# Kernel optimization log

Hardware: AMD Instinct MI355X
Metric: run time of the kernel (lower is better)

Reference implementation:

```python
import jax, jax.numpy as jnp
import numpy as np

BS, NUM_VISIT, MAX_FEAT, MAX_TARGET = 32, 6, 12, 16
NUM_FEAT, NUM_REL, HIDDEN, REDUCED, OUT = 1992, 11, 128, 256, 90
GAMMA = 0.1


def setup_inputs() -> dict:
    key = jax.random.key(0)
    ks = jax.random.split(key, 20)
    u = lambda k, shape: jax.random.uniform(k, shape, dtype=jnp.float32)
    # one/multi-hot-like dense float inputs (per docstring)
    feat_index = (u(ks[0], (BS, NUM_VISIT, MAX_FEAT, NUM_FEAT)) < 0.01).astype(jnp.float32)
    neighbor_index = (u(ks[1], (BS, NUM_VISIT, MAX_FEAT, MAX_TARGET, NUM_FEAT)) < 0.001).astype(jnp.float32)
    rel_index = (u(ks[2], (BS, NUM_VISIT, MAX_FEAT, MAX_TARGET, NUM_REL)) < 0.2).astype(jnp.float32)
    # parameters (torch.rand init in the original; xavier for embedding)
    bound = float(np.sqrt(6.0 / (NUM_FEAT + HIDDEN)))
    emb_weight = jax.random.uniform(ks[3], (NUM_FEAT, HIDDEN), dtype=jnp.float32, minval=-bound, maxval=bound)
    return {
        "feat_index": feat_index,
        "neighbor_index": neighbor_index,
        "rel_index": rel_index,
        "emb_weight": emb_weight,
        "W_edge": u(ks[4], (NUM_REL, HIDDEN)),
        "W_v": u(ks[5], (REDUCED, HIDDEN)),
        "W_r": u(ks[6], (REDUCED, HIDDEN)),
        "b_v": u(ks[7], (REDUCED,)),
        "b_r": u(ks[8], (REDUCED,)),
        "W_alpha": u(ks[9], (NUM_FEAT,)),
        "b_alpha": u(ks[10], (MAX_FEAT,)),
        "W_beta": u(ks[11], (MAX_FEAT,)),
        "b_beta": u(ks[12], (NUM_VISIT,)),
        "W_l": u(ks[13], (REDUCED, REDUCED)),
        "b_l": u(ks[14], (REDUCED,)),
        "fc_W": u(ks[15], (OUT, 2 * REDUCED)) * 0.05,
        "fc_b": u(ks[16], (OUT,)) * 0.05,
    }


def reference(feat_index, neighbor_index, rel_index, emb_weight, W_edge, W_v, W_r,
              b_v, b_r, W_alpha, b_alpha, W_beta, b_beta, W_l, b_l, fc_W, fc_b):
    num_visit = feat_index.shape[1]
    # decay buffer lamb[i] = exp(-gamma*(num_visit - i))
    lamb = jnp.exp(-GAMMA * (num_visit - jnp.arange(num_visit, dtype=feat_index.dtype)))

    # node-level attention alpha: (b,v,m)
    alpha = jax.nn.softmax(jnp.einsum('n,bvmn->bvm', W_alpha, feat_index) + b_alpha)
    # visit-level attention beta: (b,v), modulated by temporal decay
    beta = jnp.tanh(jnp.einsum('m,bvm->bv', W_beta, alpha) + b_beta) * lamb

    # reduced node embeddings: (num_feat, reduced)
    reduced_emb = emb_weight @ W_v.T + b_v
    # attention-weighted neighbor aggregation; sum over targets t fused in
    attn = alpha * beta[:, :, None]                       # (b,v,m)
    node_agg = jnp.einsum('bvm,bvmtn,nr->bvmr', attn, neighbor_index, reduced_emb)

    # reduced edge (relation) embeddings: (num_rel, reduced)
    reduced_edge = W_edge @ W_r.T + b_r
    edge_agg = jnp.einsum('bvmtr,rd->bvmd', rel_index, reduced_edge)  # sum over t fused

    agg = node_agg + edge_agg                             # (b,v,m,reduced)
    # einsum('dd, bvfd -> bvfd') in torch takes the diagonal of W_l
    h = jax.nn.relu(jnp.diagonal(W_l) * agg + b_l)        # (b,v,m,reduced)

    h_g = h.sum(axis=(1, 2))                              # (b, reduced)
    # einsum('bvmn,bvmr->bvnr').sum(n).sum(v) == contract over v,m,n
    h_p = jnp.einsum('bvm,bvmr->br', feat_index.sum(-1), h)

    z_joint = jnp.concatenate([h_g, h_p], axis=-1)        # (b, 2*reduced)
    return jax.nn.sigmoid(z_joint @ fc_W.T + fc_b)
```

## Files before the change

kernel.cpp:

```cpp
#include <hip/hip_runtime.h>
#include <math.h>

#define BS   32
#define NV   6
#define MF   12
#define MT   16
#define NF   1992
#define NR   11
#define HID  128
#define RED  256
#define OUTD 90
#define GAMMA 0.1f

#define WS_HG    0
#define WS_HP    (WS_HG + BS*RED)
#define WS_ATTN  (WS_HP + BS*RED)
#define WS_FSUM  (WS_ATTN + BS*NV*MF)
#define WS_REMB  (WS_FSUM + BS*NV*MF)
#define WS_REDGE (WS_REMB + NF*RED)
#define WS_WTV   (WS_REDGE + NR*RED)
#define WS_WTR   (WS_WTV + HID*RED)
#define WS_FCWT  (WS_WTR + HID*RED)

#define N_WTV  (HID*RED)
#define N_WTR  (HID*RED)
#define N_FCWT (2*RED*OUTD)
#define PREP_ELEMS (N_WTV + N_WTR + N_FCWT)
#define PREP_BLOCKS ((PREP_ELEMS + 255) / 256)

__global__ __launch_bounds__(256) void k_prep_attn(
        const float* __restrict__ W_v, const float* __restrict__ W_r,
        const float* __restrict__ fc_W,
        const float* __restrict__ feat, const float* __restrict__ W_alpha,
        const float* __restrict__ b_alpha, const float* __restrict__ W_beta,
        const float* __restrict__ b_beta,
        float* __restrict__ WT_v, float* __restrict__ WT_r, float* __restrict__ fcWT,
        float* __restrict__ attn_ws, float* __restrict__ fsum_ws) {
    int blk = blockIdx.x;
    int tid = threadIdx.x;
    if (blk < PREP_BLOCKS) {
        int i = blk * 256 + tid;
        if (i < N_WTV) {
            int k = i >> 8, r = i & 255;
            WT_v[i] = W_v[r * HID + k];
        } else if (i < N_WTV + N_WTR) {
            int j = i - N_WTV;
            int k = j >> 8, r = j & 255;
            WT_r[j] = W_r[r * HID + k];
        } else if (i < PREP_ELEMS) {
            int j = i - (N_WTV + N_WTR);
            int jj = j / OUTD, o = j - jj * OUTD;
            fcWT[j] = fc_W[o * (2 * RED) + jj];
        }
        return;
    }
    int bv   = blk - PREP_BLOCKS;
    int v    = bv % NV;
    int wave = tid >> 6;
    int lane = tid & 63;
    __shared__ float dot12[MF], fs12[MF];
    const float* base = feat + (size_t)bv * MF * NF;
    for (int m = wave; m < MF; m += 4) {
        const float4* rw = (const float4*)(base + (size_t)m * NF);
        const float4* wa = (const float4*)W_alpha;
        float da = 0.f, fs = 0.f;
        for (int i = lane; i < NF / 4; i += 64) {
            float4 x = rw[i];
            float4 w = wa[i];
            da += w.x * x.x + w.y * x.y + w.z * x.z + w.w * x.w;
            fs += x.x + x.y + x.z + x.w;
        }
        #pragma unroll
        for (int off = 32; off > 0; off >>= 1) {
            da += __shfl_xor(da, off);
            fs += __shfl_xor(fs, off);
        }
        if (lane == 0) { dot12[m] = da; fs12[m] = fs; }
    }
    __syncthreads();
    if (tid == 0) {
        float logits[MF];
        float mx = -1e30f;
        for (int m = 0; m < MF; ++m) { logits[m] = dot12[m] + b_alpha[m]; mx = fmaxf(mx, logits[m]); }
        float s = 0.f;
        for (int m = 0; m < MF; ++m) { logits[m] = expf(logits[m] - mx); s += logits[m]; }
        float inv = 1.f / s;
        float bdot = 0.f;
        for (int m = 0; m < MF; ++m) { logits[m] *= inv; bdot += W_beta[m] * logits[m]; }
        float lamb = expf(-GAMMA * (float)(NV - v));
        float beta = tanhf(bdot + b_beta[v]) * lamb;
        for (int m = 0; m < MF; ++m) {
            attn_ws[bv * MF + m] = logits[m] * beta;
            fsum_ws[bv * MF + m] = fs12[m];
        }
    }
}

#define NPB 4
#define NODE_BLOCKS (NF / NPB)
__global__ __launch_bounds__(256) void k_reduce(
        const float* __restrict__ emb, const float* __restrict__ W_edge,
        const float* __restrict__ WT_v, const float* __restrict__ WT_r,
        const float* __restrict__ b_v, const float* __restrict__ b_r,
        float* __restrict__ remb, float* __restrict__ redge) {
    int blk = blockIdx.x;
    int tid = threadIdx.x;
    if (blk < NODE_BLOCKS) {
        __shared__ float rows[NPB][HID];
        int n0 = blk * NPB;
        for (int i = tid; i < NPB * HID; i += 256)
            rows[i >> 7][i & 127] = emb[(size_t)n0 * HID + i];
        __syncthreads();
        float bv0 = b_v[tid];
        float a0 = bv0, a1 = bv0, a2 = bv0, a3 = bv0;
        #pragma unroll 4
        for (int k = 0; k < HID; ++k) {
            float w = WT_v[k * RED + tid];
            a0 += rows[0][k] * w;
            a1 += rows[1][k] * w;
            a2 += rows[2][k] * w;
            a3 += rows[3][k] * w;
        }
        remb[(size_t)(n0 + 0) * RED + tid] = a0;
        remb[(size_t)(n0 + 1) * RED + tid] = a1;
        remb[(size_t)(n0 + 2) * RED + tid] = a2;
        remb[(size_t)(n0 + 3) * RED + tid] = a3;
    } else {
        int e = blk - NODE_BLOCKS;
        __shared__ float row[HID];
        if (tid < HID) row[tid] = W_edge[e * HID + tid];
        __syncthreads();
        float acc = b_r[tid];
        #pragma unroll 4
        for (int k = 0; k < HID; ++k)
            acc += row[k] * WT_r[k * RED + tid];
        redge[e * RED + tid] = acc;
    }
}

#define NZCAP 1024
__global__ __launch_bounds__(256) void k_agg(
        const float* __restrict__ nbr, const float* __restrict__ rel,
        const float* __restrict__ remb, const float* __restrict__ redge,
        const float* __restrict__ attn_ws, const float* __restrict__ fsum_ws,
        const float* __restrict__ W_l, const float* __restrict__ b_l,
        float* __restrict__ h_g, float* __restrict__ h_p) {
    int bvm = blockIdx.x;
    int b   = bvm / (NV * MF);
    int tid = threadIdx.x;
    __shared__ int   nz_n[NZCAP];
    __shared__ float nz_v[NZCAP];
    __shared__ float rsum[NR];
    __shared__ int   cnt;
    if (tid == 0) cnt = 0;

    const float4* base = (const float4*)(nbr + (size_t)bvm * MT * NF);
    float4 a0 = make_float4(0.f, 0.f, 0.f, 0.f);
    float4 a1 = make_float4(0.f, 0.f, 0.f, 0.f);
    const bool has1 = (tid + 256) < (NF / 4);
    #pragma unroll 4
    for (int t = 0; t < MT; ++t) {
        const float4* r4 = base + t * (NF / 4);
        float4 x = r4[tid];
        a0.x += x.x; a0.y += x.y; a0.z += x.z; a0.w += x.w;
        if (has1) {
            float4 y = r4[tid + 256];
            a1.x += y.x; a1.y += y.y; a1.z += y.z; a1.w += y.w;
        }
    }

    if (tid < NR) {
        const float* rb = rel + (size_t)bvm * MT * NR;
        float s = 0.f;
        #pragma unroll
        for (int t = 0; t < MT; ++t) s += rb[t * NR + tid];
        rsum[tid] = s;
    }
    __syncthreads();

    {
        float vals0[4] = {a0.x, a0.y, a0.z, a0.w};
        int nb = tid * 4;
        #pragma unroll
        for (int c = 0; c < 4; ++c)
            if (vals0[c] != 0.f) {
                int p = atomicAdd(&cnt, 1);
                if (p < NZCAP) { nz_n[p] = nb + c; nz_v[p] = vals0[c]; }
            }
        if (has1) {
            float vals1[4] = {a1.x, a1.y, a1.z, a1.w};
            nb = (tid + 256) * 4;
            #pragma unroll
            for (int c = 0; c < 4; ++c)
                if (vals1[c] != 0.f) {
                    int p = atomicAdd(&cnt, 1);
                    if (p < NZCAP) { nz_n[p] = nb + c; nz_v[p] = vals1[c]; }
                }
        }
    }
    __syncthreads();

    int r = tid;
    int c = min(cnt, NZCAP);
    float node = 0.f;
    for (int i = 0; i < c; ++i)
        node += nz_v[i] * remb[(size_t)nz_n[i] * RED + r];
    float edge = 0.f;
    #pragma unroll
    for (int j = 0; j < NR; ++j)
        edge += rsum[j] * redge[j * RED + r];
    float a  = attn_ws[bvm];
    float fs = fsum_ws[bvm];
    float agg = a * node + edge;
    float h = fmaxf(0.f, W_l[(size_t)r * RED + r] * agg + b_l[r]);
    atomicAdd(&h_g[b * RED + r], h);
    atomicAdd(&h_p[b * RED + r], fs * h);
}

__global__ void k_out(const float* __restrict__ h_g, const float* __restrict__ h_p,
                      const float* __restrict__ fcWT, const float* __restrict__ fc_b,
                      float* __restrict__ out) {
    int b   = blockIdx.x;
    int tid = threadIdx.x;
    __shared__ float z[2 * RED];
    for (int j = tid; j < RED; j += 128) {
        z[j]       = h_g[b * RED + j];
        z[RED + j] = h_p[b * RED + j];
    }
    __syncthreads();
    if (tid < OUTD) {
        float acc = fc_b[tid];
        #pragma unroll 4
        for (int j = 0; j < 2 * RED; ++j)
            acc += z[j] * fcWT[j * OUTD + tid];
        out[b * OUTD + tid] = 1.f / (1.f + expf(-acc));
    }
}

extern "C" void kernel_launch(void* const* d_in, const int* in_sizes, int n_in,
                              void* d_out, int out_size, void* d_ws, size_t ws_size,
                              hipStream_t stream) {
    const float* feat    = (const float*)d_in[0];
    const float* nbr     = (const float*)d_in[1];
    const float* rel     = (const float*)d_in[2];
    const float* emb     = (const float*)d_in[3];
    const float* W_edge  = (const float*)d_in[4];
    const float* W_v     = (const float*)d_in[5];
    const float* W_r     = (const float*)d_in[6];
    const float* b_v     = (const float*)d_in[7];
    const float* b_r     = (const float*)d_in[8];
    const float* W_alpha = (const float*)d_in[9];
    const float* b_alpha = (const float*)d_in[10];
    const float* W_beta  = (const float*)d_in[11];
    const float* b_beta  = (const float*)d_in[12];
    const float* W_l     = (const float*)d_in[13];
    const float* b_l     = (const float*)d_in[14];
    const float* fc_b    = (const float*)d_in[16];
    const float* fc_W    = (const float*)d_in[15];

    float* ws    = (float*)d_ws;
    float* hg    = ws + WS_HG;
    float* hp    = ws + WS_HP;
    float* attn  = ws + WS_ATTN;
    float* fsum  = ws + WS_FSUM;
    float* remb  = ws + WS_REMB;
    float* redge = ws + WS_REDGE;
    float* WT_v  = ws + WS_WTV;
    float* WT_r  = ws + WS_WTR;
    float* fcWT  = ws + WS_FCWT;

    hipMemsetAsync(hg, 0, (size_t)2 * BS * RED * sizeof(float), stream);

    k_prep_attn<<<PREP_BLOCKS + BS * NV, 256, 0, stream>>>(
        W_v, W_r, fc_W, feat, W_alpha, b_alpha, W_beta, b_beta,
        WT_v, WT_r, fcWT, attn, fsum);
    k_reduce<<<NODE_BLOCKS + NR, 256, 0, stream>>>(
        emb, W_edge, WT_v, WT_r, b_v, b_r, remb, redge);
    k_agg<<<BS * NV * MF, 256, 0, stream>>>(
        nbr, rel, remb, redge, attn, fsum, W_l, b_l, hg, hp);
    k_out<<<BS, 128, 0, stream>>>(hg, hp, fcWT, fc_b, (float*)d_out);
}
```

Baseline: 516.9 us.

## Fold memset into prep kernel, widen reduce tiles, use nontemporal neighbor loads

Zeroing of the h_g/h_p accumulators moves into the prep kernel, which removes a separate memset launch. k_reduce now computes 8 nodes per block instead of 4, so each WT_v load is reused more often. The streaming read of the large neighbor tensor in k_agg uses nontemporal vector loads so it pollutes the cache less. k_out splits its 512-long dot product across two thread halves. Most of the runtime comes from streaming the large neighbor tensor, so these changes should matter little.

```diff
diff --git a/kernel.cpp b/kernel.cpp
--- a/kernel.cpp
+++ b/kernel.cpp
@@ -12,6 +12,8 @@
 #define OUTD 90
 #define GAMMA 0.1f
 
+typedef float f4_t __attribute__((ext_vector_type(4)));
+
 #define WS_HG    0
 #define WS_HP    (WS_HG + BS*RED)
 #define WS_ATTN  (WS_HP + BS*RED)
@@ -22,11 +24,12 @@
 #define WS_WTR   (WS_WTV + HID*RED)
 #define WS_FCWT  (WS_WTR + HID*RED)
 
+#define N_ZERO (2*BS*RED)
 #define N_WTV  (HID*RED)
 #define N_WTR  (HID*RED)
 #define N_FCWT (2*RED*OUTD)
-#define PREP_ELEMS (N_WTV + N_WTR + N_FCWT)
-#define PREP_BLOCKS ((PREP_ELEMS + 255) / 256)
+#define PREP_ELEMS (N_ZERO + N_WTV + N_WTR + N_FCWT)
+#define PREP_BLOCKS (PREP_ELEMS / 256)
 
 __global__ __launch_bounds__(256) void k_prep_attn(
         const float* __restrict__ W_v, const float* __restrict__ W_r,
@@ -34,21 +37,25 @@
         const float* __restrict__ feat, const float* __restrict__ W_alpha,
         const float* __restrict__ b_alpha, const float* __restrict__ W_beta,
         const float* __restrict__ b_beta,
+        float* __restrict__ ws_base,
         float* __restrict__ WT_v, float* __restrict__ WT_r, float* __restrict__ fcWT,
         float* __restrict__ attn_ws, float* __restrict__ fsum_ws) {
     int blk = blockIdx.x;
     int tid = threadIdx.x;
     if (blk < PREP_BLOCKS) {
         int i = blk * 256 + tid;
-        if (i < N_WTV) {
-            int k = i >> 8, r = i & 255;
-            WT_v[i] = W_v[r * HID + k];
-        } else if (i < N_WTV + N_WTR) {
-            int j = i - N_WTV;
+        if (i < N_ZERO) {
+            ws_base[i] = 0.f;
+        } else if (i < N_ZERO + N_WTV) {
+            int j = i - N_ZERO;
+            int k = j >> 8, r = j & 255;
+            WT_v[j] = W_v[r * HID + k];
+        } else if (i < N_ZERO + N_WTV + N_WTR) {
+            int j = i - (N_ZERO + N_WTV);
             int k = j >> 8, r = j & 255;
             WT_r[j] = W_r[r * HID + k];
-        } else if (i < PREP_ELEMS) {
-            int j = i - (N_WTV + N_WTR);
+        } else {
+            int j = i - (N_ZERO + N_WTV + N_WTR);
             int jj = j / OUTD, o = j - jj * OUTD;
             fcWT[j] = fc_W[o * (2 * RED) + jj];
         }
@@ -96,7 +103,7 @@
     }
 }
 
-#define NPB 4
+#define NPB 8
 #define NODE_BLOCKS (NF / NPB)
 __global__ __launch_bounds__(256) void k_reduce(
         const float* __restrict__ emb, const float* __restrict__ W_edge,
@@ -113,6 +120,7 @@
         __syncthreads();
         float bv0 = b_v[tid];
         float a0 = bv0, a1 = bv0, a2 = bv0, a3 = bv0;
+        float a4 = bv0, a5 = bv0, a6 = bv0, a7 = bv0;
         #pragma unroll 4
         for (int k = 0; k < HID; ++k) {
             float w = WT_v[k * RED + tid];
@@ -120,11 +128,14 @@
             a1 += rows[1][k] * w;
             a2 += rows[2][k] * w;
             a3 += rows[3][k] * w;
-        }
-        remb[(size_t)(n0 + 0) * RED + tid] = a0;
-        remb[(size_t)(n0 + 1) * RED + tid] = a1;
-        remb[(size_t)(n0 + 2) * RED + tid] = a2;
-        remb[(size_t)(n0 + 3) * RED + tid] = a3;
+            a4 += rows[4][k] * w;
+            a5 += rows[5][k] * w;
+            a6 += rows[6][k] * w;
+            a7 += rows[7][k] * w;
+        }
+        float* dst = remb + (size_t)n0 * RED + tid;
+        dst[0*RED] = a0; dst[1*RED] = a1; dst[2*RED] = a2; dst[3*RED] = a3;
+        dst[4*RED] = a4; dst[5*RED] = a5; dst[6*RED] = a6; dst[7*RED] = a7;
     } else {
         int e = blk - NODE_BLOCKS;
         __shared__ float row[HID];
@@ -154,18 +165,18 @@
     __shared__ int   cnt;
     if (tid == 0) cnt = 0;
 
-    const float4* base = (const float4*)(nbr + (size_t)bvm * MT * NF);
-    float4 a0 = make_float4(0.f, 0.f, 0.f, 0.f);
-    float4 a1 = make_float4(0.f, 0.f, 0.f, 0.f);
+    const f4_t* base = (const f4_t*)(nbr + (size_t)bvm * MT * NF);
+    f4_t a0 = (f4_t)(0.f);
+    f4_t a1 = (f4_t)(0.f);
     const bool has1 = (tid + 256) < (NF / 4);
     #pragma unroll 4
     for (int t = 0; t < MT; ++t) {
-        const float4* r4 = base + t * (NF / 4);
-        float4 x = r4[tid];
-        a0.x += x.x; a0.y += x.y; a0.z += x.z; a0.w += x.w;
+        const f4_t* r4 = base + t * (NF / 4);
+        f4_t x = __builtin_nontemporal_load(r4 + tid);
+        a0 += x;
         if (has1) {
-            float4 y = r4[tid + 256];
-            a1.x += y.x; a1.y += y.y; a1.z += y.z; a1.w += y.w;
+            f4_t y = __builtin_nontemporal_load(r4 + tid + 256);
+            a1 += y;
         }
     }
 
@@ -179,22 +190,20 @@
     __syncthreads();
 
     {
-        float vals0[4] = {a0.x, a0.y, a0.z, a0.w};
         int nb = tid * 4;
         #pragma unroll
         for (int c = 0; c < 4; ++c)
-            if (vals0[c] != 0.f) {
+            if (a0[c] != 0.f) {
                 int p = atomicAdd(&cnt, 1);
-                if (p < NZCAP) { nz_n[p] = nb + c; nz_v[p] = vals0[c]; }
+                if (p < NZCAP) { nz_n[p] = nb + c; nz_v[p] = a0[c]; }
             }
         if (has1) {
-            float vals1[4] = {a1.x, a1.y, a1.z, a1.w};
             nb = (tid + 256) * 4;
             #pragma unroll
             for (int c = 0; c < 4; ++c)
-                if (vals1[c] != 0.f) {
+                if (a1[c] != 0.f) {
                     int p = atomicAdd(&cnt, 1);
-                    if (p < NZCAP) { nz_n[p] = nb + c; nz_v[p] = vals1[c]; }
+                    if (p < NZCAP) { nz_n[p] = nb + c; nz_v[p] = a1[c]; }
                 }
         }
     }
@@ -217,22 +226,31 @@
     atomicAdd(&h_p[b * RED + r], fs * h);
 }
 
-__global__ void k_out(const float* __restrict__ h_g, const float* __restrict__ h_p,
-                      const float* __restrict__ fcWT, const float* __restrict__ fc_b,
-                      float* __restrict__ out) {
+__global__ __launch_bounds__(256) void k_out(
+        const float* __restrict__ h_g, const float* __restrict__ h_p,
+        const float* __restrict__ fcWT, const float* __restrict__ fc_b,
+        float* __restrict__ out) {
     int b   = blockIdx.x;
     int tid = threadIdx.x;
     __shared__ float z[2 * RED];
-    for (int j = tid; j < RED; j += 128) {
+    __shared__ float part[2][OUTD];
+    for (int j = tid; j < RED; j += 256) {
         z[j]       = h_g[b * RED + j];
         z[RED + j] = h_p[b * RED + j];
     }
     __syncthreads();
+    int o = tid & 127, half = tid >> 7;
+    if (o < OUTD) {
+        float acc = 0.f;
+        int j0 = half * RED;
+        #pragma unroll 8
+        for (int j = j0; j < j0 + RED; ++j)
+            acc += z[j] * fcWT[j * OUTD + o];
+        part[half][o] = acc;
+    }
+    __syncthreads();
     if (tid < OUTD) {
-        float acc = fc_b[tid];
-        #pragma unroll 4
-        for (int j = 0; j < 2 * RED; ++j)
-            acc += z[j] * fcWT[j * OUTD + tid];
+        float acc = part[0][tid] + part[1][tid] + fc_b[tid];
         out[b * OUTD + tid] = 1.f / (1.f + expf(-acc));
     }
 }
@@ -255,8 +273,8 @@
     const float* b_beta  = (const float*)d_in[12];
     const float* W_l     = (const float*)d_in[13];
     const float* b_l     = (const float*)d_in[14];
+    const float* fc_W    = (const float*)d_in[15];
     const float* fc_b    = (const float*)d_in[16];
-    const float* fc_W    = (const float*)d_in[15];
 
     float* ws    = (float*)d_ws;
     float* hg    = ws + WS_HG;
@@ -269,14 +287,12 @@
     float* WT_r  = ws + WS_WTR;
     float* fcWT  = ws + WS_FCWT;
 
-    hipMemsetAsync(hg, 0, (size_t)2 * BS * RED * sizeof(float), stream);
-
     k_prep_attn<<<PREP_BLOCKS + BS * NV, 256, 0, stream>>>(
         W_v, W_r, fc_W, feat, W_alpha, b_alpha, W_beta, b_beta,
-        WT_v, WT_r, fcWT, attn, fsum);
+        ws, WT_v, WT_r, fcWT, attn, fsum);
     k_reduce<<<NODE_BLOCKS + NR, 256, 0, stream>>>(
         emb, W_edge, WT_v, WT_r, b_v, b_r, remb, redge);
     k_agg<<<BS * NV * MF, 256, 0, stream>>>(
         nbr, rel, remb, redge, attn, fsum, W_l, b_l, hg, hp);
-    k_out<<<BS, 128, 0, stream>>>(hg, hp, fcWT, fc_b, (float*)d_out);
-}
+    k_out<<<BS, 256, 0, stream>>>(hg, hp, fcWT, fc_b, (float*)d_out);
+}
```

Result: faster. 454.5 us (-12.1%).
